# Optimization experiments

Measured on AMD Instinct MI355X. Metric: run time of the kernel, lower is better.

Reference implementation:

```python
import jax, jax.numpy as jnp
import numpy as np

# db4 analysis filters (pywt.Wavelet('db4').dec_lo / dec_hi)
_DEC_LO = np.array([-0.010597401784997278, 0.032883011666982945, 0.030841381835986965,
                    -0.18703481171888114, -0.02798376941698385, 0.6308807679295904,
                    0.7148465705525415, 0.23037781330885523], dtype=np.float32)
_DEC_HI = np.array([-0.23037781330885523, 0.7148465705525415, -0.6308807679295904,
                    -0.02798376941698385, 0.18703481171888114, 0.030841381835986965,
                    -0.032883011666982945, -0.010597401784997278], dtype=np.float32)
# pytorch_wavelets stores filters reversed (torch conv = correlation); lax.conv is
# also correlation, so use the same reversed filters. Shape [2, 1, L].
_H = jnp.asarray(np.stack([_DEC_LO[::-1], _DEC_HI[::-1]])[:, None, :])

B, SW, SWS, HW, K, J = 2048, 4, 64, 8, 128, 3
DWT_LEN = 84  # 14 (lo, level 3) + 35 (hi1) + 21 (hi2) + 14 (hi3)


def _dwt_level(x, h):
    """One analysis level, mode='reflect' (pytorch_wavelets afb1d). x: [M, N]."""
    N = x.shape[-1]
    L = h.shape[-1]
    outsize = (N + L - 1) // 2          # pywt.dwt_coeff_len, non-periodization
    p = 2 * (outsize - 1) - N + L
    if p % 2 == 1:                       # odd total pad: one extra zero at the end
        x = jnp.pad(x, ((0, 0), (0, 1)))
    x = jnp.pad(x, ((0, 0), (p // 2, p // 2)), mode='reflect')
    y = jax.lax.conv_general_dilated(x[:, None, :], h, (2,), 'VALID')  # [M, 2, out]
    return y[:, 0, :], y[:, 1, :]


def setup_inputs() -> dict:
    key = jax.random.key(0)
    k1, k2, k3 = jax.random.split(key, 3)
    x = jax.random.normal(k1, (B, 1, SW * SWS, HW, HW), dtype=jnp.float32)
    # one Conv3d(1 -> K, kernel=(DWT_LEN, 8, 8)) per subwindow, kaiming-ish init
    fan_in = DWT_LEN * HW * HW
    conv_weight = jax.random.normal(k2, (SW, K, DWT_LEN, HW, HW), dtype=jnp.float32) / np.sqrt(fan_in)
    conv_bias = jax.random.normal(k3, (SW, K), dtype=jnp.float32) * 0.01
    return {"x": x, "conv_weight": conv_weight, "conv_bias": conv_bias}


def reference(x, conv_weight, conv_bias):
    b = x.shape[0]
    # [B,1,T,8,8] -> [B,SW,8,8,SWS]: DWT runs along the time axis of each subwindow
    xt = x[:, 0].reshape(b, SW, SWS, HW, HW).transpose(0, 1, 3, 4, 2)
    xm = xt.reshape(-1, SWS)  # [B*SW*64, 64]
    lo, highs = xm, []
    for _ in range(J):
        lo, hi = _dwt_level(lo, _H)
        highs.append(hi)
    coeffs = jnp.concatenate([lo] + highs, axis=-1)  # [M, 84], order: lo, hi1, hi2, hi3
    c = coeffs.reshape(b, SW, HW, HW, DWT_LEN).transpose(0, 1, 4, 2, 3)  # [B,SW,84,8,8]
    # per-subwindow Conv3d that fully reduces (t,h,w) -> [B, SW, K]
    feat = jnp.einsum('bsthw,skthw->bsk', c, conv_weight) + conv_bias[None]
    # Dropout3d is identity in eval; LeakyReLU default slope 0.01 (typo in source
    # means leakyrelu_negative_slope is never applied)
    return jax.nn.leaky_relu(feat, 0.01).reshape(b, SW * K)
```

## Files before the change

### kernel.cpp

```cpp
#include <hip/hip_runtime.h>
#include <stdint.h>

typedef unsigned int   u32;
typedef unsigned short u16;
typedef __bf16 bf16x8 __attribute__((ext_vector_type(8)));
typedef float  f32x4  __attribute__((ext_vector_type(4)));

struct WdT { float v[84][64]; };

constexpr WdT build_wd() {
    WdT W{};
    const float GLc[8] = { 0.23037781330885523f,  0.7148465705525415f,
                           0.6308807679295904f,  -0.02798376941698385f,
                          -0.18703481171888114f,  0.030841381835986965f,
                           0.032883011666982945f,-0.010597401784997278f };
    const float GHc[8] = {-0.010597401784997278f,-0.032883011666982945f,
                           0.030841381835986965f, 0.18703481171888114f,
                          -0.02798376941698385f, -0.6308807679295904f,
                           0.7148465705525415f,  -0.23037781330885523f };
    for (int j = 0; j < 64; ++j) {
        float lo1[35] = {}, lo2[21] = {};
        for (int i = 0; i < 35; ++i) {
            float sl = 0.f, sh = 0.f;
            for (int t = 0; t < 8; ++t) {
                int s = 2*i + t - 6;
                if (s < 0)   s = -s;
                if (s >= 64) s = 126 - s;
                if (s == j) { sl += GLc[t]; sh += GHc[t]; }
            }
            lo1[i] = sl; W.v[14 + i][j] = sh;
        }
        for (int i = 0; i < 21; ++i) {
            float sl = 0.f, sh = 0.f;
            for (int t = 0; t < 8; ++t) {
                int s = 2*i + t - 6;
                if (s < 0)   s = -s;
                if (s >= 36) s = 70 - s;
                if (s < 35) { sl += lo1[s]*GLc[t]; sh += lo1[s]*GHc[t]; }
            }
            lo2[i] = sl; W.v[49 + i][j] = sh;
        }
        for (int i = 0; i < 14; ++i) {
            float sl = 0.f, sh = 0.f;
            for (int t = 0; t < 8; ++t) {
                int s = 2*i + t - 6;
                if (s < 0)   s = -s;
                if (s >= 22) s = 42 - s;
                if (s < 21) { sl += lo2[s]*GLc[t]; sh += lo2[s]*GHc[t]; }
            }
            W.v[i][j] = sl; W.v[70 + i][j] = sh;
        }
    }
    return W;
}

__constant__ WdT WD = build_wd();

__device__ inline u16 f32_bf16(float f) {
    u32 u = __float_as_uint(f);
    u += 0x7fffu + ((u >> 16) & 1u);
    return (u16)(u >> 16);
}
__device__ inline u32 pack2_bf16(float a, float b) {
    u32 ua = __float_as_uint(a); ua += 0x7fffu + ((ua >> 16) & 1u);
    u32 ub = __float_as_uint(b); ub += 0x7fffu + ((ub >> 16) & 1u);
    return (ua >> 16) | (ub & 0xffff0000u);
}

typedef const __attribute__((address_space(1))) u32 gas_u32;
typedef __attribute__((address_space(3)))       u32 las_u32;
__device__ inline void gl16(const void* g, void* l) {
    __builtin_amdgcn_global_load_lds((gas_u32*)g, (las_u32*)l, 16, 0, 0);
}

__global__ __launch_bounds__(256) void fold_w(const float* __restrict__ cw,
                                              u16* __restrict__ Wf) {
    const int tid = threadIdx.x;
    const int sk  = blockIdx.x;
    const int s   = sk >> 7;
    const int n   = sk & 127;
    const int hw  = tid & 63;
    const int tg  = __builtin_amdgcn_readfirstlane((int)(tid >> 6));
    const int t0  = tg * 16;
    const float* wk = cw + (size_t)sk * (84 * 64);

    float acc[16];
#pragma unroll
    for (int j = 0; j < 16; ++j) acc[j] = 0.f;

#pragma unroll 4
    for (int tau = 0; tau < 84; ++tau) {
        const float wv = wk[tau * 64 + hw];
#pragma unroll
        for (int j = 0; j < 16; ++j) acc[j] += wv * WD.v[tau][t0 + j];
    }

    const int nt  = n >> 4;
    const int fr  = n & 15;
    const int fq  = (hw >> 3) & 3;
    const int jj  = hw & 7;
    const int kbh = hw >> 5;
#pragma unroll
    for (int j = 0; j < 16; ++j) {
        const int t = t0 + j;
        const size_t idx =
            ((((size_t)(s * 128 + t * 2 + kbh)) * 8 + nt) * 64 + fq * 16 + fr) * 8 + jj;
        Wf[idx] = f32_bf16(acc[j]);
    }
}

template <int KQ>
__global__ __launch_bounds__(256) void gemm_f(const float* __restrict__ X,
                                              const u16* __restrict__ Wf,
                                              float* __restrict__ P) {
    constexpr int NSTEP = 128 / KQ;
    __shared__ float As[2][4096];
    __shared__ u16   Bs[2][4096];

    const int tid  = threadIdx.x;
    const int lane = tid & 63;
    const int w    = tid >> 6;
    const int wm   = w >> 1, wn = w & 1;
    const int fr   = lane & 15;
    const int fq   = lane >> 4;

    const int bid  = blockIdx.x;
    const int wg   = (bid & 7) * (8 * KQ) + (bid >> 3);
    const int mt   = wg & 15;
    const int s    = (wg >> 4) & 3;
    const int kq   = wg >> 6;

    const int am   = tid >> 3;
    const int ab   = ((tid & 7) * 16) ^ ((am & 7) << 4);
    const float* xa = X + (size_t)(mt * 128 + am) * 16384 + s * 4096
                        + (size_t)kq * (4096 / KQ) + (ab >> 2);
    const char* wb0 = (const char*)Wf + ((size_t)(s * 128 + kq * NSTEP) << 13)
                        + (size_t)tid * 16;

    f32x4 acc[4][4];
#pragma unroll
    for (int mi = 0; mi < 4; ++mi)
#pragma unroll
        for (int ni = 0; ni < 4; ++ni) acc[mi][ni] = (f32x4){0.f, 0.f, 0.f, 0.f};

#define STAGE(buf, step)                                                       \
    do {                                                                       \
        char* la = (char*)&As[buf][0] + tid * 16;                              \
        char* lb = (char*)&Bs[buf][0] + tid * 16;                              \
        const float* ga = xa + (size_t)(step) * 32;                            \
        const char*  gb = wb0 + ((size_t)(step) << 13);                        \
        gl16(ga,            la);                                               \
        gl16(ga + 524288,   la + 4096);                                        \
        gl16(ga + 1048576,  la + 8192);                                        \
        gl16(ga + 1572864,  la + 12288);                                       \
        gl16(gb,            lb);                                               \
        gl16(gb + 4096,     lb + 4096);                                        \
    } while (0)

    STAGE(0, 0);
    int cur = 0;
#pragma unroll 1
    for (int step = 0; step < NSTEP; ++step) {
        if (step + 1 < NSTEP) {
            STAGE(cur ^ 1, step + 1);
            asm volatile("s_waitcnt vmcnt(6)" ::: "memory");
        } else {
            asm volatile("s_waitcnt vmcnt(0)" ::: "memory");
        }
        __builtin_amdgcn_s_barrier();

        const float* Ab = &As[cur][0];
        const u16*   Bb = &Bs[cur][0];
        bf16x8 bfr[4];
#pragma unroll
        for (int ni = 0; ni < 4; ++ni)
            bfr[ni] = *reinterpret_cast<const bf16x8*>(
                Bb + ((wn * 4 + ni) * 64 + lane) * 8);
        const int swz = (fr & 7) << 4;
        const int b0  = (fq * 32) ^ swz;
        const int b1  = (fq * 32 + 16) ^ swz;
#pragma unroll
        for (int mi = 0; mi < 4; ++mi) {
            const int m = wm * 64 + mi * 16 + fr;
            const f32x4 r0 = *reinterpret_cast<const f32x4*>(Ab + m * 32 + (b0 >> 2));
            const f32x4 r1 = *reinterpret_cast<const f32x4*>(Ab + m * 32 + (b1 >> 2));
            union { u32 u[4]; bf16x8 v; } av;
            av.u[0] = pack2_bf16(r0.x, r0.y); av.u[1] = pack2_bf16(r0.z, r0.w);
            av.u[2] = pack2_bf16(r1.x, r1.y); av.u[3] = pack2_bf16(r1.z, r1.w);
#pragma unroll
            for (int ni = 0; ni < 4; ++ni)
                acc[mi][ni] = __builtin_amdgcn_mfma_f32_16x16x32_bf16(
                    av.v, bfr[ni], acc[mi][ni], 0, 0, 0);
        }
        asm volatile("s_waitcnt lgkmcnt(0)" ::: "memory");
        __builtin_amdgcn_s_barrier();
        cur ^= 1;
    }
#undef STAGE

    float* pg = P + (size_t)kq * (2048 * 512)
                  + (size_t)(mt * 128 + wm * 64) * 512 + s * 128 + wn * 64 + fr;
#pragma unroll
    for (int mi = 0; mi < 4; ++mi)
#pragma unroll
        for (int ni = 0; ni < 4; ++ni)
#pragma unroll
            for (int r = 0; r < 4; ++r)
                pg[(size_t)(mi * 16 + fq * 4 + r) * 512 + ni * 16] = acc[mi][ni][r];
}

__global__ __launch_bounds__(256) void reduce_k(const float* __restrict__ P,
                                                const float* __restrict__ bias,
                                                float* __restrict__ out, int nks) {
    const int t = blockIdx.x * 256 + threadIdx.x;
    const size_t base = (size_t)t * 4;
    f32x4 sum = {0.f, 0.f, 0.f, 0.f};
    for (int k = 0; k < nks; ++k)
        sum += *reinterpret_cast<const f32x4*>(P + (size_t)k * (2048 * 512) + base);
    const f32x4 b = *reinterpret_cast<const f32x4*>(bias + (base & 511));
    f32x4 o = sum + b;
    o.x = o.x > 0.f ? o.x : 0.01f * o.x;
    o.y = o.y > 0.f ? o.y : 0.01f * o.y;
    o.z = o.z > 0.f ? o.z : 0.01f * o.z;
    o.w = o.w > 0.f ? o.w : 0.01f * o.w;
    __builtin_nontemporal_store(o, reinterpret_cast<f32x4*>(out + base));
}

extern "C" void kernel_launch(void* const* d_in, const int* in_sizes, int n_in,
                              void* d_out, int out_size, void* d_ws, size_t ws_size,
                              hipStream_t stream) {
    const float* x  = (const float*)d_in[0];
    const float* cw = (const float*)d_in[1];
    const float* cb = (const float*)d_in[2];
    float* out = (float*)d_out;

    u16*   Wf = (u16*)d_ws;
    float* P  = (float*)((char*)d_ws + (4u << 20));

    const size_t MN = (size_t)2048 * 512 * 4;
    fold_w<<<512, 256, 0, stream>>>(cw, Wf);
    if (ws_size >= (4u << 20) + 8 * MN) {
        gemm_f<8><<<512, 256, 0, stream>>>(x, Wf, P);
        reduce_k<<<1024, 256, 0, stream>>>(P, cb, out, 8);
    } else {
        gemm_f<4><<<256, 256, 0, stream>>>(x, Wf, P);
        reduce_k<<<1024, 256, 0, stream>>>(P, cb, out, 4);
    }
}
```

Baseline: 233.8 us.

## Shrink GEMM tile to 64 rows, use 512-thread blocks and triple buffering

```diff
diff --git a/kernel.cpp b/kernel.cpp
--- a/kernel.cpp
+++ b/kernel.cpp
@@ -110,103 +110,94 @@
 }
 
 template <int KQ>
-__global__ __launch_bounds__(256) void gemm_f(const float* __restrict__ X,
-                                              const u16* __restrict__ Wf,
-                                              float* __restrict__ P) {
-    constexpr int NSTEP = 128 / KQ;
-    __shared__ float As[2][4096];
-    __shared__ u16   Bs[2][4096];
+__global__ __launch_bounds__(512, 6) void gemm_f(const float* __restrict__ X,
+                                                 const u16* __restrict__ Wf,
+                                                 float* __restrict__ P) {
+    constexpr int NSTEP = (4096 / KQ) / 32;
+    __shared__ float As[3][2048];
+    __shared__ u16   Bs[3][4096];
 
     const int tid  = threadIdx.x;
     const int lane = tid & 63;
     const int w    = tid >> 6;
-    const int wm   = w >> 1, wn = w & 1;
+    const int wm   = w >> 1;
+    const int wn   = w & 1;
     const int fr   = lane & 15;
     const int fq   = lane >> 4;
 
     const int bid  = blockIdx.x;
-    const int wg   = (bid & 7) * (8 * KQ) + (bid >> 3);
-    const int mt   = wg & 15;
-    const int s    = (wg >> 4) & 3;
-    const int kq   = wg >> 6;
+    const int wg   = (bid & 7) * (16 * KQ) + (bid >> 3);
+    const int mt   = wg & 31;
+    const int s    = (wg >> 5) & 3;
+    const int kq   = wg >> 7;
 
     const int am   = tid >> 3;
     const int ab   = ((tid & 7) * 16) ^ ((am & 7) << 4);
-    const float* xa = X + (size_t)(mt * 128 + am) * 16384 + s * 4096
+    const float* xa = X + (size_t)(mt * 64 + am) * 16384 + s * 4096
                         + (size_t)kq * (4096 / KQ) + (ab >> 2);
     const char* wb0 = (const char*)Wf + ((size_t)(s * 128 + kq * NSTEP) << 13)
                         + (size_t)tid * 16;
 
-    f32x4 acc[4][4];
-#pragma unroll
-    for (int mi = 0; mi < 4; ++mi)
-#pragma unroll
-        for (int ni = 0; ni < 4; ++ni) acc[mi][ni] = (f32x4){0.f, 0.f, 0.f, 0.f};
+    f32x4 acc[4];
+#pragma unroll
+    for (int ni = 0; ni < 4; ++ni) acc[ni] = (f32x4){0.f, 0.f, 0.f, 0.f};
 
 #define STAGE(buf, step)                                                       \
     do {                                                                       \
-        char* la = (char*)&As[buf][0] + tid * 16;                              \
-        char* lb = (char*)&Bs[buf][0] + tid * 16;                              \
-        const float* ga = xa + (size_t)(step) * 32;                            \
-        const char*  gb = wb0 + ((size_t)(step) << 13);                        \
-        gl16(ga,            la);                                               \
-        gl16(ga + 524288,   la + 4096);                                        \
-        gl16(ga + 1048576,  la + 8192);                                        \
-        gl16(ga + 1572864,  la + 12288);                                       \
-        gl16(gb,            lb);                                               \
-        gl16(gb + 4096,     lb + 4096);                                        \
+        gl16(xa + (size_t)(step) * 32, (char*)&As[buf][0] + tid * 16);         \
+        gl16(wb0 + ((size_t)(step) << 13), (char*)&Bs[buf][0] + tid * 16);     \
     } while (0)
 
     STAGE(0, 0);
-    int cur = 0;
-#pragma unroll 1
+    STAGE(1, 1);
+
+#pragma unroll
     for (int step = 0; step < NSTEP; ++step) {
-        if (step + 1 < NSTEP) {
-            STAGE(cur ^ 1, step + 1);
-            asm volatile("s_waitcnt vmcnt(6)" ::: "memory");
+        const int buf = step % 3;
+        if (step + 2 < NSTEP) {
+            STAGE((step + 2) % 3, step + 2);
+            asm volatile("s_waitcnt vmcnt(4)" ::: "memory");
+        } else if (step + 2 == NSTEP) {
+            asm volatile("s_waitcnt vmcnt(2)" ::: "memory");
         } else {
             asm volatile("s_waitcnt vmcnt(0)" ::: "memory");
         }
         __builtin_amdgcn_s_barrier();
 
-        const float* Ab = &As[cur][0];
-        const u16*   Bb = &Bs[cur][0];
+        const float* Ab = &As[buf][0];
+        const u16*   Bb = &Bs[buf][0];
         bf16x8 bfr[4];
 #pragma unroll
         for (int ni = 0; ni < 4; ++ni)
             bfr[ni] = *reinterpret_cast<const bf16x8*>(
                 Bb + ((wn * 4 + ni) * 64 + lane) * 8);
+
+        const int m   = wm * 16 + fr;
         const int swz = (fr & 7) << 4;
         const int b0  = (fq * 32) ^ swz;
         const int b1  = (fq * 32 + 16) ^ swz;
-#pragma unroll
-        for (int mi = 0; mi < 4; ++mi) {
-            const int m = wm * 64 + mi * 16 + fr;
-            const f32x4 r0 = *reinterpret_cast<const f32x4*>(Ab + m * 32 + (b0 >> 2));
-            const f32x4 r1 = *reinterpret_cast<const f32x4*>(Ab + m * 32 + (b1 >> 2));
-            union { u32 u[4]; bf16x8 v; } av;
-            av.u[0] = pack2_bf16(r0.x, r0.y); av.u[1] = pack2_bf16(r0.z, r0.w);
-            av.u[2] = pack2_bf16(r1.x, r1.y); av.u[3] = pack2_bf16(r1.z, r1.w);
-#pragma unroll
-            for (int ni = 0; ni < 4; ++ni)
-                acc[mi][ni] = __builtin_amdgcn_mfma_f32_16x16x32_bf16(
-                    av.v, bfr[ni], acc[mi][ni], 0, 0, 0);
-        }
+        const f32x4 r0 = *reinterpret_cast<const f32x4*>(Ab + m * 32 + (b0 >> 2));
+        const f32x4 r1 = *reinterpret_cast<const f32x4*>(Ab + m * 32 + (b1 >> 2));
+        union { u32 u[4]; bf16x8 v; } av;
+        av.u[0] = pack2_bf16(r0.x, r0.y); av.u[1] = pack2_bf16(r0.z, r0.w);
+        av.u[2] = pack2_bf16(r1.x, r1.y); av.u[3] = pack2_bf16(r1.z, r1.w);
+#pragma unroll
+        for (int ni = 0; ni < 4; ++ni)
+            acc[ni] = __builtin_amdgcn_mfma_f32_16x16x32_bf16(av.v, bfr[ni],
+                                                              acc[ni], 0, 0, 0);
+
         asm volatile("s_waitcnt lgkmcnt(0)" ::: "memory");
         __builtin_amdgcn_s_barrier();
-        cur ^= 1;
     }
 #undef STAGE
 
     float* pg = P + (size_t)kq * (2048 * 512)
-                  + (size_t)(mt * 128 + wm * 64) * 512 + s * 128 + wn * 64 + fr;
-#pragma unroll
-    for (int mi = 0; mi < 4; ++mi)
-#pragma unroll
-        for (int ni = 0; ni < 4; ++ni)
-#pragma unroll
-            for (int r = 0; r < 4; ++r)
-                pg[(size_t)(mi * 16 + fq * 4 + r) * 512 + ni * 16] = acc[mi][ni][r];
+                  + (size_t)(mt * 64 + wm * 16) * 512 + s * 128 + wn * 64 + fr;
+#pragma unroll
+    for (int ni = 0; ni < 4; ++ni)
+#pragma unroll
+        for (int r = 0; r < 4; ++r)
+            pg[(size_t)(fq * 4 + r) * 512 + ni * 16] = acc[ni][r];
 }
 
 __global__ __launch_bounds__(256) void reduce_k(const float* __restrict__ P,
@@ -240,10 +231,10 @@
     const size_t MN = (size_t)2048 * 512 * 4;
     fold_w<<<512, 256, 0, stream>>>(cw, Wf);
     if (ws_size >= (4u << 20) + 8 * MN) {
-        gemm_f<8><<<512, 256, 0, stream>>>(x, Wf, P);
+        gemm_f<8><<<1024, 512, 0, stream>>>(x, Wf, P);
         reduce_k<<<1024, 256, 0, stream>>>(P, cb, out, 8);
     } else {
-        gemm_f<4><<<256, 256, 0, stream>>>(x, Wf, P);
+        gemm_f<4><<<512, 512, 0, stream>>>(x, Wf, P);
         reduce_k<<<1024, 256, 0, stream>>>(P, cb, out, 4);
     }
 }
```

After: 235.6 us. Within noise of the previous version (+0.8%).

## Switch GEMM to 32x32x16 bf16 MFMA with per-wave 32-row tiles

Applied to the files above, without the earlier changes.

```diff
diff --git a/kernel.cpp b/kernel.cpp
--- a/kernel.cpp
+++ b/kernel.cpp
@@ -5,6 +5,7 @@
 typedef unsigned short u16;
 typedef __bf16 bf16x8 __attribute__((ext_vector_type(8)));
 typedef float  f32x4  __attribute__((ext_vector_type(4)));
+typedef float  f32x16 __attribute__((ext_vector_type(16)));
 
 struct WdT { float v[84][64]; };
 
@@ -95,34 +96,34 @@
         for (int j = 0; j < 16; ++j) acc[j] += wv * WD.v[tau][t0 + j];
     }
 
-    const int nt  = n >> 4;
-    const int fr  = n & 15;
-    const int fq  = (hw >> 3) & 3;
-    const int jj  = hw & 7;
-    const int kbh = hw >> 5;
-#pragma unroll
-    for (int j = 0; j < 16; ++j) {
-        const int t = t0 + j;
+    const int kh = (hw >> 4) & 1;
+    const int hb = (hw >> 3) & 1;
+    const int jj = hw & 7;
+    const int nt = n >> 5;
+    const int lb = hb * 32 + (n & 31);
+#pragma unroll
+    for (int js = 0; js < 16; ++js) {
+        const int sigma = t0 + js;
+        const int kb = sigma * 2 + (hw >> 5);
         const size_t idx =
-            ((((size_t)(s * 128 + t * 2 + kbh)) * 8 + nt) * 64 + fq * 16 + fr) * 8 + jj;
-        Wf[idx] = f32_bf16(acc[j]);
+            ((((size_t)(s * 128 + kb) * 2 + kh) * 4 + nt) * 512) + lb * 8 + jj;
+        Wf[idx] = f32_bf16(acc[js]);
     }
 }
 
 template <int KQ>
-__global__ __launch_bounds__(256) void gemm_f(const float* __restrict__ X,
-                                              const u16* __restrict__ Wf,
-                                              float* __restrict__ P) {
-    constexpr int NSTEP = 128 / KQ;
+__global__ __launch_bounds__(256, 2) void gemm_f(const float* __restrict__ X,
+                                                 const u16* __restrict__ Wf,
+                                                 float* __restrict__ P) {
+    constexpr int NSTEP = (4096 / KQ) / 32;
     __shared__ float As[2][4096];
     __shared__ u16   Bs[2][4096];
 
     const int tid  = threadIdx.x;
     const int lane = tid & 63;
     const int w    = tid >> 6;
-    const int wm   = w >> 1, wn = w & 1;
-    const int fr   = lane & 15;
-    const int fq   = lane >> 4;
+    const int col  = lane & 31;
+    const int hi   = lane >> 5;
 
     const int bid  = blockIdx.x;
     const int wg   = (bid & 7) * (8 * KQ) + (bid >> 3);
@@ -130,83 +131,83 @@
     const int s    = (wg >> 4) & 3;
     const int kq   = wg >> 6;
 
-    const int am   = tid >> 3;
-    const int ab   = ((tid & 7) * 16) ^ ((am & 7) << 4);
+    const int am = tid >> 3;
+    const int ab = ((tid & 7) * 16) ^ ((am & 7) << 4);
     const float* xa = X + (size_t)(mt * 128 + am) * 16384 + s * 4096
-                        + (size_t)kq * (4096 / KQ) + (ab >> 2);
-    const char* wb0 = (const char*)Wf + ((size_t)(s * 128 + kq * NSTEP) << 13)
+                        + kq * (4096 / KQ) + (ab >> 2);
+    const char* wb0 = (const char*)Wf + (size_t)(s * 128 + kq * NSTEP) * 8192
                         + (size_t)tid * 16;
 
-    f32x4 acc[4][4];
-#pragma unroll
-    for (int mi = 0; mi < 4; ++mi)
-#pragma unroll
-        for (int ni = 0; ni < 4; ++ni) acc[mi][ni] = (f32x4){0.f, 0.f, 0.f, 0.f};
-
-#define STAGE(buf, step)                                                       \
+    f32x16 acc[4];
+#pragma unroll
+    for (int nt = 0; nt < 4; ++nt)
+#pragma unroll
+        for (int e = 0; e < 16; ++e) acc[nt][e] = 0.f;
+
+#define STAGE(buf, st)                                                         \
     do {                                                                       \
         char* la = (char*)&As[buf][0] + tid * 16;                              \
-        char* lb = (char*)&Bs[buf][0] + tid * 16;                              \
-        const float* ga = xa + (size_t)(step) * 32;                            \
-        const char*  gb = wb0 + ((size_t)(step) << 13);                        \
-        gl16(ga,            la);                                               \
-        gl16(ga + 524288,   la + 4096);                                        \
-        gl16(ga + 1048576,  la + 8192);                                        \
-        gl16(ga + 1572864,  la + 12288);                                       \
-        gl16(gb,            lb);                                               \
-        gl16(gb + 4096,     lb + 4096);                                        \
+        const float* ga = xa + (size_t)(st) * 32;                              \
+        gl16(ga,               la);                                            \
+        gl16(ga + 32 * 16384,  la + 4096);                                     \
+        gl16(ga + 64 * 16384,  la + 8192);                                     \
+        gl16(ga + 96 * 16384,  la + 12288);                                    \
+        const char* gb = wb0 + (size_t)(st) * 8192;                            \
+        char*       lb = (char*)&Bs[buf][0] + tid * 16;                        \
+        gl16(gb,        lb);                                                   \
+        gl16(gb + 4096, lb + 4096);                                            \
     } while (0)
 
     STAGE(0, 0);
-    int cur = 0;
-#pragma unroll 1
+
+    const int m  = w * 32 + col;
+    const int m7 = col & 7;
+#pragma unroll 2
     for (int step = 0; step < NSTEP; ++step) {
+        const int buf = step & 1;
         if (step + 1 < NSTEP) {
-            STAGE(cur ^ 1, step + 1);
+            STAGE(buf ^ 1, step + 1);
             asm volatile("s_waitcnt vmcnt(6)" ::: "memory");
         } else {
             asm volatile("s_waitcnt vmcnt(0)" ::: "memory");
         }
         __builtin_amdgcn_s_barrier();
 
-        const float* Ab = &As[cur][0];
-        const u16*   Bb = &Bs[cur][0];
-        bf16x8 bfr[4];
-#pragma unroll
-        for (int ni = 0; ni < 4; ++ni)
-            bfr[ni] = *reinterpret_cast<const bf16x8*>(
-                Bb + ((wn * 4 + ni) * 64 + lane) * 8);
-        const int swz = (fr & 7) << 4;
-        const int b0  = (fq * 32) ^ swz;
-        const int b1  = (fq * 32 + 16) ^ swz;
-#pragma unroll
-        for (int mi = 0; mi < 4; ++mi) {
-            const int m = wm * 64 + mi * 16 + fr;
-            const f32x4 r0 = *reinterpret_cast<const f32x4*>(Ab + m * 32 + (b0 >> 2));
-            const f32x4 r1 = *reinterpret_cast<const f32x4*>(Ab + m * 32 + (b1 >> 2));
+        const char* Ab = (const char*)&As[buf][0];
+        const u16*  Bb = &Bs[buf][0];
+#pragma unroll
+        for (int kh = 0; kh < 2; ++kh) {
+            const int c = kh * 4 + hi * 2;
+            const f32x4 r0 = *reinterpret_cast<const f32x4*>(
+                Ab + m * 128 + (((c    ) ^ m7) << 4));
+            const f32x4 r1 = *reinterpret_cast<const f32x4*>(
+                Ab + m * 128 + (((c + 1) ^ m7) << 4));
             union { u32 u[4]; bf16x8 v; } av;
             av.u[0] = pack2_bf16(r0.x, r0.y); av.u[1] = pack2_bf16(r0.z, r0.w);
             av.u[2] = pack2_bf16(r1.x, r1.y); av.u[3] = pack2_bf16(r1.z, r1.w);
 #pragma unroll
-            for (int ni = 0; ni < 4; ++ni)
-                acc[mi][ni] = __builtin_amdgcn_mfma_f32_16x16x32_bf16(
-                    av.v, bfr[ni], acc[mi][ni], 0, 0, 0);
-        }
+            for (int nt = 0; nt < 4; ++nt) {
+                const bf16x8 bf = *reinterpret_cast<const bf16x8*>(
+                    Bb + ((kh * 4 + nt) * 64 + lane) * 8);
+                acc[nt] = __builtin_amdgcn_mfma_f32_32x32x16_bf16(
+                    av.v, bf, acc[nt], 0, 0, 0);
+            }
+        }
+
         asm volatile("s_waitcnt lgkmcnt(0)" ::: "memory");
         __builtin_amdgcn_s_barrier();
-        cur ^= 1;
     }
 #undef STAGE
 
     float* pg = P + (size_t)kq * (2048 * 512)
-                  + (size_t)(mt * 128 + wm * 64) * 512 + s * 128 + wn * 64 + fr;
-#pragma unroll
-    for (int mi = 0; mi < 4; ++mi)
-#pragma unroll
-        for (int ni = 0; ni < 4; ++ni)
+                  + (size_t)(mt * 128 + w * 32 + hi * 4) * 512 + s * 128 + col;
+#pragma unroll
+    for (int nt = 0; nt < 4; ++nt)
+#pragma unroll
+        for (int q = 0; q < 4; ++q)
 #pragma unroll
             for (int r = 0; r < 4; ++r)
-                pg[(size_t)(mi * 16 + fq * 4 + r) * 512 + ni * 16] = acc[mi][ni][r];
+                pg[(size_t)(q * 8 + r) * 512 + nt * 32] = acc[nt][q * 4 + r];
 }
 
 __global__ __launch_bounds__(256) void reduce_k(const float* __restrict__ P,
```

After: 233.2 us. About the same (-0.3%).
